# Kernel tuning notes

Hardware: AMD Instinct MI355X
Metric: run time of the kernel (lower is better)

Reference implementation:

```python
import jax, jax.numpy as jnp
import numpy as np

N = 40000          # nodes
E = 400000         # edges (avg degree 10)
MUL0, MUL1 = 64, 32   # 64x0e + 32x1o
RAD, HID = 8, 64      # fc_neurons = [8, 64]
WNUM = 192            # tp.weight_numel = 64+64+32+32
NUM_NEIGHBORS = 10.0
INV3 = 1.0 / np.sqrt(3.0)   # wigner coeff for 1o x 1o -> 0e


def _lin(s, v, Ws, Wv, attr):
    """FullyConnectedTensorProduct(x, 1x0e attr) == per-irrep linear, fan-in normalized."""
    out_s = (s @ Ws) * attr * (1.0 / np.sqrt(Ws.shape[0]))
    out_v = jnp.einsum('nud,uv->nvd', v, Wv) * attr[..., None] * (1.0 / np.sqrt(Wv.shape[0]))
    return out_s, out_v


def setup_inputs() -> dict:
    key = jax.random.key(0)
    ks = jax.random.split(key, 16)
    return {
        'node_input':   jax.random.normal(ks[0], (N, MUL0 + 3 * MUL1), jnp.float32),
        'node_attr':    jnp.ones((N, 1), jnp.float32),
        'edge_attr':    jax.random.normal(ks[1], (E, 4), jnp.float32),   # 1x0e + 1x1o
        'edge_scalars': jax.random.uniform(ks[2], (E, RAD), jnp.float32),
        'W_sc_s': jax.random.normal(ks[3], (MUL0, MUL0), jnp.float32),
        'W_sc_v': jax.random.normal(ks[4], (MUL1, MUL1), jnp.float32),
        'W1_s':   jax.random.normal(ks[5], (MUL0, MUL0), jnp.float32),
        'W1_v':   jax.random.normal(ks[6], (MUL1, MUL1), jnp.float32),
        'W2_s':   jax.random.normal(ks[7], (MUL0 + MUL1, MUL0), jnp.float32),
        'W2_v':   jax.random.normal(ks[8], (MUL0 + MUL1, MUL1), jnp.float32),
        'W3':     jax.random.normal(ks[9], (MUL0 + MUL1, 1), jnp.float32),
        'fcW1':   jax.random.normal(ks[10], (RAD, HID), jnp.float32),
        'fcW2':   jax.random.normal(ks[11], (HID, WNUM), jnp.float32),
        'edge_src': jax.random.randint(ks[12], (E,), 0, N, jnp.int32),
        'edge_dst': jax.random.randint(ks[13], (E,), 0, N, jnp.int32),
    }


def reference(node_input, node_attr, edge_attr, edge_scalars,
              W_sc_s, W_sc_v, W1_s, W1_v, W2_s, W2_v, W3, fcW1, fcW2,
              edge_src, edge_dst):
    n = node_input.shape[0]
    s_in = node_input[:, :MUL0]                       # (N, 64)   0e
    v_in = node_input[:, MUL0:].reshape(n, MUL1, 3)   # (N, 32,3) 1o

    # self connection + first linear (FCTP with 1x0e attr)
    sc_s, sc_v = _lin(s_in, v_in, W_sc_s, W_sc_v, node_attr)
    f_s,  f_v  = _lin(s_in, v_in, W1_s,  W1_v,  node_attr)

    # radial MLP -> per-edge tensor-product weights (silu, fan-in normalized)
    h = jax.nn.silu(edge_scalars @ fcW1 * (1.0 / np.sqrt(RAD)))
    w = h @ fcW2 * (1.0 / np.sqrt(HID))               # (E, 192)
    wA, wB, wC, wD = w[:, :64], w[:, 64:128], w[:, 128:160], w[:, 160:192]

    # gather source node features
    xs = f_s[edge_src]                                # (E, 64)
    xv = f_v[edge_src]                                # (E, 32, 3)
    y0 = edge_attr[:, :1]                             # (E, 1)  0e
    y1 = edge_attr[:, 1:4]                            # (E, 3)  1o

    # 'uvu' tensor-product paths -> irreps_mid = 64x0e + 32x0e + 64x1o + 32x1o
    outA = wA * xs * y0                                            # 0e x 0e -> 0e
    outD = wD * jnp.einsum('eud,ed->eu', xv, y1) * INV3            # 1o x 1o -> 0e
    outB = wB[:, :, None] * xs[:, :, None] * y1[:, None, :]       # 0e x 1o -> 1o
    outC = wC[:, :, None] * xv * y0[:, :, None]                    # 1o x 0e -> 1o
    edge_feat = jnp.concatenate(
        [outA, outD, outB.reshape(-1, MUL0 * 3), outC.reshape(-1, MUL1 * 3)], axis=1)  # (E, 384)

    # scatter_add into destination nodes, normalized by sqrt(num_neighbors)
    agg = jax.ops.segment_sum(edge_feat, edge_dst, num_segments=n)
    agg = agg * (1.0 / np.sqrt(NUM_NEIGHBORS))

    ms = agg[:, :MUL0 + MUL1]                               # (N, 96)   0e
    mv = agg[:, MUL0 + MUL1:].reshape(n, MUL0 + MUL1, 3)    # (N, 96,3) 1o

    # lin2: mid -> output ; lin3: mid -> 0e (scalars only)
    c_s, c_v = _lin(ms, mv, W2_s, W2_v, node_attr)
    conv = jnp.concatenate([c_s, c_v.reshape(n, -1)], axis=1)
    sc   = jnp.concatenate([sc_s, sc_v.reshape(n, -1)], axis=1)
    angle = 0.1 * (ms @ W3) * node_attr * (1.0 / np.sqrt(MUL0 + MUL1))  # (N, 1)

    # sc.output_mask is all-ones here (every output irrep has a path)
    cos, sin = jnp.cos(angle), jnp.sin(angle)
    return cos * sc + sin * conv
```

## Files before the change

kernel.cpp:

```cpp
#include <hip/hip_runtime.h>
#include <math.h>

#define MUL0 64
#define MUL1 32
#define RADF 8
#define HIDF 64
#define WNUM 192
#define NODE_F 160
#define AGG_F  384

#define INV_SQRT64 0.125f
#define INV_SQRT32 0.17677669529663687f
#define INV_SQRT8  0.35355339059327373f
#define INV_SQRT96 0.10206207261596575f
#define INV_SQRT10 0.31622776601683794f
#define INV_SQRT3  0.5773502691896258f

typedef __attribute__((ext_vector_type(8))) short bf16x8;
typedef __attribute__((ext_vector_type(4))) float f32x4;

__device__ __forceinline__ float bf2f(unsigned short u) {
    return __uint_as_float((unsigned)u << 16);
}
__device__ __forceinline__ unsigned short f2bfu(float x) {
    unsigned ua = __float_as_uint(x);
    return (unsigned short)((ua + 0x7FFF + ((ua >> 16) & 1)) >> 16);
}
__device__ __forceinline__ unsigned bf16pack(float a, float b) {
    unsigned ua = __float_as_uint(a);
    unsigned ub = __float_as_uint(b);
    ua = (ua + 0x7FFF + ((ua >> 16) & 1)) >> 16;
    ub = (ub + 0x7FFF + ((ub >> 16) & 1)) >> 16;
    return ua | (ub << 16);
}
__device__ __forceinline__ int rdlane(int v, int i) {
    return __builtin_amdgcn_readlane(v, i);
}
__device__ __forceinline__ float rdlanef(float v, int i) {
    return __int_as_float(__builtin_amdgcn_readlane(__float_as_int(v), i));
}
__device__ __forceinline__ bf16x8 cvt8(float4 a, float4 b) {
    union { unsigned q[4]; bf16x8 v; } r;
    r.q[0] = bf16pack(a.x, a.y);
    r.q[1] = bf16pack(a.z, a.w);
    r.q[2] = bf16pack(b.x, b.y);
    r.q[3] = bf16pack(b.z, b.w);
    return r.v;
}

__global__ __launch_bounds__(256) void k_node_lin(
    const float* __restrict__ node_input,
    const float* __restrict__ node_attr,
    const float* __restrict__ W1_s,
    const float* __restrict__ W1_v,
    float* __restrict__ f, int N)
{
    __shared__ unsigned short s_w1s[8 * 64 * 8];
    __shared__ unsigned short s_w1v[4 * 32 * 8];
    int tid = threadIdx.x;

    for (int task = tid; task < 8 * 64; task += 256) {
        int col = task & 63, koct = task >> 6;
        const float* wp = W1_s + (size_t)(koct * 8) * MUL0 + col;
        unsigned pk0 = bf16pack(wp[0 * MUL0] * INV_SQRT64, wp[1 * MUL0] * INV_SQRT64);
        unsigned pk1 = bf16pack(wp[2 * MUL0] * INV_SQRT64, wp[3 * MUL0] * INV_SQRT64);
        unsigned pk2 = bf16pack(wp[4 * MUL0] * INV_SQRT64, wp[5 * MUL0] * INV_SQRT64);
        unsigned pk3 = bf16pack(wp[6 * MUL0] * INV_SQRT64, wp[7 * MUL0] * INV_SQRT64);
        *(uint4*)&s_w1s[task * 8] = make_uint4(pk0, pk1, pk2, pk3);
    }
    for (int task = tid; task < 4 * 32; task += 256) {
        int col = task & 31, koct = task >> 5;
        const float* wp = W1_v + (size_t)(koct * 8) * MUL1 + col;
        unsigned pk0 = bf16pack(wp[0 * MUL1] * INV_SQRT32, wp[1 * MUL1] * INV_SQRT32);
        unsigned pk1 = bf16pack(wp[2 * MUL1] * INV_SQRT32, wp[3 * MUL1] * INV_SQRT32);
        unsigned pk2 = bf16pack(wp[4 * MUL1] * INV_SQRT32, wp[5 * MUL1] * INV_SQRT32);
        unsigned pk3 = bf16pack(wp[6 * MUL1] * INV_SQRT32, wp[7 * MUL1] * INV_SQRT32);
        *(uint4*)&s_w1v[task * 8] = make_uint4(pk0, pk1, pk2, pk3);
    }
    __syncthreads();

    int lane = tid & 63;
    int wv = tid >> 6;
    int l15 = lane & 15, lh = lane >> 4;
    int ntiles = (N + 15) >> 4;

    for (int tile = blockIdx.x * 4 + wv; tile < ntiles; tile += gridDim.x * 4) {
        int n0 = tile << 4;
        int m = min(16, N - n0);
        int nrow = n0 + min(l15, m - 1);
        const float* inn = node_input + (size_t)nrow * NODE_F;

        float attr[4];
        #pragma unroll
        for (int r = 0; r < 4; ++r)
            attr[r] = node_attr[n0 + min(lh * 4 + r, m - 1)];

        bf16x8 inS[2];
        #pragma unroll
        for (int kk = 0; kk < 2; ++kk) {
            const float* p0 = inn + kk * 32 + lh * 8;
            inS[kk] = cvt8(*(const float4*)p0, *(const float4*)(p0 + 4));
        }
        #pragma unroll
        for (int cb = 0; cb < 4; ++cb) {
            f32x4 a = {0.f, 0.f, 0.f, 0.f};
            #pragma unroll
            for (int kk = 0; kk < 2; ++kk) {
                bf16x8 b = *(const bf16x8*)&s_w1s[(((kk * 4 + lh) * 64) + cb * 16 + l15) * 8];
                a = __builtin_amdgcn_mfma_f32_16x16x32_bf16(inS[kk], b, a, 0, 0, 0);
            }
            #pragma unroll
            for (int r = 0; r < 4; ++r) {
                int node = lh * 4 + r;
                if (node < m)
                    f[(size_t)(n0 + node) * NODE_F + cb * 16 + l15] = a[r] * attr[r];
            }
        }

        #pragma unroll
        for (int d = 0; d < 3; ++d) {
            float t[8];
            #pragma unroll
            for (int j = 0; j < 8; ++j)
                t[j] = inn[64 + (lh * 8 + j) * 3 + d];
            bf16x8 inV = cvt8(make_float4(t[0], t[1], t[2], t[3]),
                              make_float4(t[4], t[5], t[6], t[7]));
            #pragma unroll
            for (int cb = 0; cb < 2; ++cb) {
                bf16x8 b = *(const bf16x8*)&s_w1v[((lh * 32) + cb * 16 + l15) * 8];
                f32x4 a = {0.f, 0.f, 0.f, 0.f};
                a = __builtin_amdgcn_mfma_f32_16x16x32_bf16(inV, b, a, 0, 0, 0);
                #pragma unroll
                for (int r = 0; r < 4; ++r) {
                    int node = lh * 4 + r;
                    if (node < m)
                        f[(size_t)(n0 + node) * NODE_F + 64 + d * 32 + cb * 16 + l15] =
                            a[r] * attr[r];
                }
            }
        }
    }
}

__global__ void k_count(const int* __restrict__ edge_dst, int* deg, int E)
{
    int e = blockIdx.x * blockDim.x + threadIdx.x;
    if (e < E) atomicAdd(&deg[edge_dst[e]], 1);
}

__global__ __launch_bounds__(1024) void k_scan(const int* __restrict__ deg,
                                               int* __restrict__ off,
                                               int* __restrict__ cur, int N)
{
    __shared__ int swsum[16];
    __shared__ int swoff[16];
    __shared__ int sbase;
    __shared__ int stotal;
    int lane = threadIdx.x & 63, wid = threadIdx.x >> 6;
    if (threadIdx.x == 0) sbase = 0;
    __syncthreads();
    int ngroups = N >> 2;
    for (int base = 0; base < ngroups; base += 1024) {
        int g = base + threadIdx.x;
        int4 v = make_int4(0, 0, 0, 0);
        if (g < ngroups) v = ((const int4*)deg)[g];
        int s = v.x + v.y + v.z + v.w;
        int val = s;
        #pragma unroll
        for (int sh = 1; sh < 64; sh <<= 1) {
            int t = __shfl_up(val, sh);
            if (lane >= sh) val += t;
        }
        if (lane == 63) swsum[wid] = val;
        __syncthreads();
        if (threadIdx.x < 16) {
            int x = swsum[threadIdx.x];
            int xv = x;
            #pragma unroll
            for (int sh = 1; sh < 16; sh <<= 1) {
                int t = __shfl_up(xv, sh);
                if ((int)threadIdx.x >= sh) xv += t;
            }
            swoff[threadIdx.x] = xv - x;
            if (threadIdx.x == 15) stotal = xv;
        }
        __syncthreads();
        if (g < ngroups) {
            int b = sbase + swoff[wid] + (val - s);
            int4 o;
            o.x = b; o.y = b + v.x; o.z = o.y + v.y; o.w = o.z + v.z;
            ((int4*)off)[g] = o;
            ((int4*)cur)[g] = o;
        }
        __syncthreads();
        if (threadIdx.x == 0) sbase += stotal;
        __syncthreads();
    }
    if (threadIdx.x == 0) {
        int b = sbase;
        for (int i = (ngroups << 2); i < N; ++i) { off[i] = b; cur[i] = b; b += deg[i]; }
        off[N] = b;
    }
}

__global__ void k_scatter(const int* __restrict__ edge_dst,
                          int* cur, int* __restrict__ csr, int E)
{
    int e = blockIdx.x * blockDim.x + threadIdx.x;
    if (e < E) {
        int d = edge_dst[e];
        int pos = atomicAdd(&cur[d], 1);
        csr[pos] = e;
    }
}

#define FLUSH_AGG(node)                                              \
    do {                                                             \
        float* an = agg + (size_t)(node) * AGG_F;                    \
        atomicAdd(&an[lane], accA);                                  \
        atomicAdd(&an[96  + lane], accB0);                           \
        atomicAdd(&an[192 + lane], accB1);                           \
        atomicAdd(&an[288 + lane], accB2);                           \
        if (lane < 32) {                                             \
            atomicAdd(&an[160 + u], accX0);                          \
            atomicAdd(&an[256 + u], accX1);                          \
            atomicAdd(&an[352 + u], accX2);                          \
        } else {                                                     \
            atomicAdd(&an[64 + u], accX0);                           \
        }                                                            \
    } while (0)

__global__ __launch_bounds__(256, 3) void k_edge_fused(
    const float* __restrict__ f,
    const float* __restrict__ edge_scalars,
    const float* __restrict__ edge_attr,
    const float* __restrict__ fcW1,
    const float* __restrict__ fcW2,
    const int* __restrict__ edge_src,
    const int* __restrict__ edge_dst,
    const int* __restrict__ csr,
    float* agg, int E)
{
    __shared__ unsigned short s_w2t[8 * 192 * 8];
    __shared__ unsigned short s_w[4][16 * 216];
    __shared__ float s_fcW1[512];

    int tid  = threadIdx.x;
    int lane = tid & 63;
    int wv   = tid >> 6;
    int l15  = lane & 15, lh = lane >> 4;
    int u    = lane & 31;

    for (int task = tid; task < 1536; task += 256) {
        int col = task % 192, oct = task / 192;
        const float* wp = fcW2 + (size_t)(oct * 8) * WNUM + col;
        unsigned pk0 = bf16pack(wp[0 * WNUM], wp[1 * WNUM]);
        unsigned pk1 = bf16pack(wp[2 * WNUM], wp[3 * WNUM]);
        unsigned pk2 = bf16pack(wp[4 * WNUM], wp[5 * WNUM]);
        unsigned pk3 = bf16pack(wp[6 * WNUM], wp[7 * WNUM]);
        *(uint4*)&s_w2t[oct * 1536 + col * 8] = make_uint4(pk0, pk1, pk2, pk3);
    }
    for (int i = tid; i < 512; i += 256)
        s_fcW1[i] = fcW1[i];
    __syncthreads();

    unsigned short* sw = s_w[wv];
    int nwt = (E + 15) >> 4;
    int stride4 = gridDim.x * 4;

    int wt = blockIdx.x * 4 + wv;
    if (wt >= nwt) return;

    int P = wt << 4;
    int m = min(16, E - P);
    int e0 = csr[P + min(l15, m - 1)];
    int src = edge_src[e0];
    int dst = edge_dst[e0];
    float4 ea = *(const float4*)(edge_attr + (size_t)e0 * 4);
    float4 es0, es1;
    {
        const float4* esp = (const float4*)(edge_scalars + (size_t)e0 * RADF);
        es0 = esp[0]; es1 = esp[1];
    }

    while (true) {
        int wt_n = wt + stride4;
        bool hn = wt_n < nwt;
        int P_n = hn ? (wt_n << 4) : 0;
        int m_n = hn ? min(16, E - P_n) : 1;

        int e_n = csr[hn ? (P_n + min(l15, m_n - 1)) : 0];

        float xs[16], xv0[16], xv1[16], xv2[16];
        #pragma unroll
        for (int i = 0; i < 16; ++i) {
            int si = rdlane(src, i);
            const float* fb = f + (size_t)si * NODE_F;
            xs[i]  = fb[lane];
            xv0[i] = fb[64 + u];
            xv1[i] = fb[96 + u];
            xv2[i] = fb[128 + u];
        }

        float es[8] = {es0.x, es0.y, es0.z, es0.w, es1.x, es1.y, es1.z, es1.w};
        union { unsigned q[4]; bf16x8 v; } A0, A1;
        #pragma unroll
        for (int jp = 0; jp < 4; ++jp) {
            int k0 = lh * 8 + 2 * jp;
            float aL0 = 0.f, aL1 = 0.f, aH0 = 0.f, aH1 = 0.f;
            #pragma unroll
            for (int r = 0; r < 8; ++r) {
                float2 wl = *(const float2*)&s_fcW1[r * 64 + k0];
                float2 wh = *(const float2*)&s_fcW1[r * 64 + 32 + k0];
                aL0 = fmaf(es[r], wl.x, aL0);
                aL1 = fmaf(es[r], wl.y, aL1);
                aH0 = fmaf(es[r], wh.x, aH0);
                aH1 = fmaf(es[r], wh.y, aH1);
            }
            aL0 *= INV_SQRT8; aL1 *= INV_SQRT8; aH0 *= INV_SQRT8; aH1 *= INV_SQRT8;
            aL0 = aL0 / (1.f + __expf(-aL0));
            aL1 = aL1 / (1.f + __expf(-aL1));
            aH0 = aH0 / (1.f + __expf(-aH0));
            aH1 = aH1 / (1.f + __expf(-aH1));
            A0.q[jp] = bf16pack(aL0, aL1);
            A1.q[jp] = bf16pack(aH0, aH1);
        }

        int src_n = edge_src[e_n];
        int dst_n = edge_dst[e_n];
        float4 ea_n = *(const float4*)(edge_attr + (size_t)e_n * 4);
        float4 es0_n, es1_n;
        {
            const float4* espn = (const float4*)(edge_scalars + (size_t)e_n * RADF);
            es0_n = espn[0]; es1_n = espn[1];
        }

        #pragma unroll
        for (int cb = 0; cb < 12; ++cb) {
            bf16x8 b0 = *(const bf16x8*)&s_w2t[ lh      * 1536 + (cb * 16 + l15) * 8];
            bf16x8 b1 = *(const bf16x8*)&s_w2t[(4 + lh) * 1536 + (cb * 16 + l15) * 8];
            f32x4 acc = {0.f, 0.f, 0.f, 0.f};
            acc = __builtin_amdgcn_mfma_f32_16x16x32_bf16(A0.v, b0, acc, 0, 0, 0);
            acc = __builtin_amdgcn_mfma_f32_16x16x32_bf16(A1.v, b1, acc, 0, 0, 0);
            #pragma unroll
            for (int r = 0; r < 4; ++r)
                sw[(lh * 4 + r) * 216 + cb * 16 + l15] = f2bfu(acc[r] * INV_SQRT64);
        }

        float accA = 0.f, accB0 = 0.f, accB1 = 0.f, accB2 = 0.f;
        float accX0 = 0.f, accX1 = 0.f, accX2 = 0.f;
        int curd = rdlane(dst, 0);
        #pragma unroll
        for (int i = 0; i < 16; ++i) {
            if (i < m) {
                int di = rdlane(dst, i);
                if (di != curd) {
                    FLUSH_AGG(curd);
                    accA = accB0 = accB1 = accB2 = 0.f;
                    accX0 = accX1 = accX2 = 0.f;
                    curd = di;
                }
                float eax = rdlanef(ea.x, i);
                float eay = rdlanef(ea.y, i);
                float eaz = rdlanef(ea.z, i);
                float eaw = rdlanef(ea.w, i);
                float W0 = bf2f(sw[i * 216 + lane]);
                float W1 = bf2f(sw[i * 216 + 64 + lane]);
                float W2 = bf2f(sw[i * 216 + 128 + lane]);
                accA = fmaf(W0 * xs[i], eax, accA);
                float bx = W1 * xs[i];
                accB0 = fmaf(bx, eay, accB0);
                accB1 = fmaf(bx, eaz, accB1);
                accB2 = fmaf(bx, eaw, accB2);
                if (lane < 32) {
                    float cc = W2 * eax;
                    accX0 = fmaf(cc, xv0[i], accX0);
                    accX1 = fmaf(cc, xv1[i], accX1);
                    accX2 = fmaf(cc, xv2[i], accX2);
                } else {
                    float dv = xv0[i] * eay + xv1[i] * eaz + xv2[i] * eaw;
                    accX0 = fmaf(W2 * INV_SQRT3, dv, accX0);
                }
            }
        }
        FLUSH_AGG(curd);

        if (!hn) break;
        wt = wt_n; P = P_n; m = m_n;
        src = src_n; dst = dst_n; ea = ea_n; es0 = es0_n; es1 = es1_n;
    }
}

__global__ __launch_bounds__(256) void k_out(
    const float* __restrict__ node_input,
    const float* __restrict__ node_attr,
    const float* __restrict__ agg,
    const float* __restrict__ W_sc_s,
    const float* __restrict__ W_sc_v,
    const float* __restrict__ W2_s,
    const float* __restrict__ W2_v,
    const float* __restrict__ W3,
    float* __restrict__ out, int N)
{
    __shared__ unsigned short s_w2s[12 * 64 * 8];
    __shared__ unsigned short s_wss[ 8 * 64 * 8];
    __shared__ unsigned short s_w2v[12 * 32 * 8];
    __shared__ unsigned short s_wsv[ 4 * 32 * 8];
    __shared__ unsigned short s_w3 [12 * 16 * 8];

    const float pre = INV_SQRT10 * INV_SQRT96;
    int tid = threadIdx.x;

    for (int task = tid; task < 12 * 64; task += 256) {
        int col = task & 63, koct = task >> 6;
        const float* wp = W2_s + (size_t)(koct * 8) * MUL0 + col;
        unsigned pk0 = bf16pack(wp[0 * MUL0] * pre, wp[1 * MUL0] * pre);
        unsigned pk1 = bf16pack(wp[2 * MUL0] * pre, wp[3 * MUL0] * pre);
        unsigned pk2 = bf16pack(wp[4 * MUL0] * pre, wp[5 * MUL0] * pre);
        unsigned pk3 = bf16pack(wp[6 * MUL0] * pre, wp[7 * MUL0] * pre);
        *(uint4*)&s_w2s[task * 8] = make_uint4(pk0, pk1, pk2, pk3);
    }
    for (int task = tid; task < 8 * 64; task += 256) {
        int col = task & 63, koct = task >> 6;
        const float* wp = W_sc_s + (size_t)(koct * 8) * MUL0 + col;
        unsigned pk0 = bf16pack(wp[0 * MUL0] * INV_SQRT64, wp[1 * MUL0] * INV_SQRT64);
        unsigned pk1 = bf16pack(wp[2 * MUL0] * INV_SQRT64, wp[3 * MUL0] * INV_SQRT64);
        unsigned pk2 = bf16pack(wp[4 * MUL0] * INV_SQRT64, wp[5 * MUL0] * INV_SQRT64);
        unsigned pk3 = bf16pack(wp[6 * MUL0] * INV_SQRT64, wp[7 * MUL0] * INV_SQRT64);
        *(uint4*)&s_wss[task * 8] = make_uint4(pk0, pk1, pk2, pk3);
    }
    for (int task = tid; task < 12 * 32; task += 256) {
        int col = task & 31, koct = task >> 5;
        const float* wp = W2_v + (size_t)(koct * 8) * MUL1 + col;
        unsigned pk0 = bf16pack(wp[0 * MUL1] * pre, wp[1 * MUL1] * pre);
        unsigned pk1 = bf16pack(wp[2 * MUL1] * pre, wp[3 * MUL1] * pre);
        unsigned pk2 = bf16pack(wp[4 * MUL1] * pre, wp[5 * MUL1] * pre);
        unsigned pk3 = bf16pack(wp[6 * MUL1] * pre, wp[7 * MUL1] * pre);
        *(uint4*)&s_w2v[task * 8] = make_uint4(pk0, pk1, pk2, pk3);
    }
    for (int task = tid; task < 4 * 32; task += 256) {
        int col = task & 31, koct = task >> 5;
        const float* wp = W_sc_v + (size_t)(koct * 8) * MUL1 + col;
        unsigned pk0 = bf16pack(wp[0 * MUL1] * INV_SQRT32, wp[1 * MUL1] * INV_SQRT32);
        unsigned pk1 = bf16pack(wp[2 * MUL1] * INV_SQRT32, wp[3 * MUL1] * INV_SQRT32);
        unsigned pk2 = bf16pack(wp[4 * MUL1] * INV_SQRT32, wp[5 * MUL1] * INV_SQRT32);
        unsigned pk3 = bf16pack(wp[6 * MUL1] * INV_SQRT32, wp[7 * MUL1] * INV_SQRT32);
        *(uint4*)&s_wsv[task * 8] = make_uint4(pk0, pk1, pk2, pk3);
    }
    for (int task = tid; task < 12 * 16; task += 256) {
        int col = task & 15, koct = task >> 4;
        const float sc3 = 0.1f * pre;
        unsigned pk0 = 0, pk1 = 0, pk2 = 0, pk3 = 0;
        if (col == 0) {
            const float* wp = W3 + koct * 8;
            pk0 = bf16pack(wp[0] * sc3, wp[1] * sc3);
            pk1 = bf16pack(wp[2] * sc3, wp[3] * sc3);
            pk2 = bf16pack(wp[4] * sc3, wp[5] * sc3);
            pk3 = bf16pack(wp[6] * sc3, wp[7] * sc3);
        }
        *(uint4*)&s_w3[task * 8] = make_uint4(pk0, pk1, pk2, pk3);
    }
    __syncthreads();

    int lane = tid & 63;
    int wv = tid >> 6;
    int l15 = lane & 15, lh = lane >> 4;
    int ntiles = (N + 15) >> 4;

    for (int tile = blockIdx.x * 4 + wv; tile < ntiles; tile += gridDim.x * 4) {
        int n0 = tile << 4;
        int m = min(16, N - n0);
        int nrow = n0 + min(l15, m - 1);
        const float* agn = agg + (size_t)nrow * AGG_F;
        const float* inn = node_input + (size_t)nrow * NODE_F;

        bf16x8 aggA[3], inS[2];
        #pragma unroll
        for (int kk = 0; kk < 3; ++kk) {
            const float* p0 = agn + kk * 32 + lh * 8;
            aggA[kk] = cvt8(*(const float4*)p0, *(const float4*)(p0 + 4));
        }
        #pragma unroll
        for (int kk = 0; kk < 2; ++kk) {
            const float* p0 = inn + kk * 32 + lh * 8;
            inS[kk] = cvt8(*(const float4*)p0, *(const float4*)(p0 + 4));
        }

        f32x4 convS[4], scS[4], angD = {0.f, 0.f, 0.f, 0.f};
        #pragma unroll
        for (int cb = 0; cb < 4; ++cb) {
            f32x4 a = {0.f, 0.f, 0.f, 0.f};
            #pragma unroll
            for (int kk = 0; kk < 3; ++kk) {
                bf16x8 b = *(const bf16x8*)&s_w2s[(((kk * 4 + lh) * 64) + cb * 16 + l15) * 8];
                a = __builtin_amdgcn_mfma_f32_16x16x32_bf16(aggA[kk], b, a, 0, 0, 0);
            }
            convS[cb] = a;
            f32x4 s = {0.f, 0.f, 0.f, 0.f};
            #pragma unroll
            for (int kk = 0; kk < 2; ++kk) {
                bf16x8 b = *(const bf16x8*)&s_wss[(((kk * 4 + lh) * 64) + cb * 16 + l15) * 8];
                s = __builtin_amdgcn_mfma_f32_16x16x32_bf16(inS[kk], b, s, 0, 0, 0);
            }
            scS[cb] = s;
        }
        #pragma unroll
        for (int kk = 0; kk < 3; ++kk) {
            bf16x8 b = *(const bf16x8*)&s_w3[(((kk * 4 + lh) * 16) + l15) * 8];
            angD = __builtin_amdgcn_mfma_f32_16x16x32_bf16(aggA[kk], b, angD, 0, 0, 0);
        }

        float attr[4], cs[4], sn[4];
        #pragma unroll
        for (int r = 0; r < 4; ++r) {
            attr[r] = node_attr[n0 + min(lh * 4 + r, m - 1)];
            float ang = __shfl(angD[r], lane & 48) * attr[r];
            cs[r] = cosf(ang);
            sn[r] = sinf(ang);
        }

        #pragma unroll
        for (int cb = 0; cb < 4; ++cb)
            #pragma unroll
            for (int r = 0; r < 4; ++r) {
                int node = lh * 4 + r;
                if (node < m)
                    out[(size_t)(n0 + node) * NODE_F + cb * 16 + l15] =
                        attr[r] * (cs[r] * scS[cb][r] + sn[r] * convS[cb][r]);
            }

        #pragma unroll
        for (int d = 0; d < 3; ++d) {
            bf16x8 aggV[3], inV;
            #pragma unroll
            for (int kk = 0; kk < 3; ++kk) {
                const float* p0 = agn + 96 + d * 96 + kk * 32 + lh * 8;
                aggV[kk] = cvt8(*(const float4*)p0, *(const float4*)(p0 + 4));
            }
            {
                float t[8];
                #pragma unroll
                for (int j = 0; j < 8; ++j)
                    t[j] = inn[64 + (lh * 8 + j) * 3 + d];
                inV = cvt8(make_float4(t[0], t[1], t[2], t[3]),
                           make_float4(t[4], t[5], t[6], t[7]));
            }
            #pragma unroll
            for (int cb = 0; cb < 2; ++cb) {
                f32x4 a = {0.f, 0.f, 0.f, 0.f};
                #pragma unroll
                for (int kk = 0; kk < 3; ++kk) {
                    bf16x8 b = *(const bf16x8*)&s_w2v[(((kk * 4 + lh) * 32) + cb * 16 + l15) * 8];
                    a = __builtin_amdgcn_mfma_f32_16x16x32_bf16(aggV[kk], b, a, 0, 0, 0);
                }
                f32x4 s = {0.f, 0.f, 0.f, 0.f};
                {
                    bf16x8 b = *(const bf16x8*)&s_wsv[((lh * 32) + cb * 16 + l15) * 8];
                    s = __builtin_amdgcn_mfma_f32_16x16x32_bf16(inV, b, s, 0, 0, 0);
                }
                #pragma unroll
                for (int r = 0; r < 4; ++r) {
                    int node = lh * 4 + r;
                    if (node < m)
                        out[(size_t)(n0 + node) * NODE_F + 64 + (cb * 16 + l15) * 3 + d] =
                            attr[r] * (cs[r] * s[r] + sn[r] * a[r]);
                }
            }
        }
    }
}

extern "C" void kernel_launch(void* const* d_in, const int* in_sizes, int n_in,
                              void* d_out, int out_size, void* d_ws, size_t ws_size,
                              hipStream_t stream)
{
    const float* node_input   = (const float*)d_in[0];
    const float* node_attr    = (const float*)d_in[1];
    const float* edge_attr    = (const float*)d_in[2];
    const float* edge_scalars = (const float*)d_in[3];
    const float* W_sc_s       = (const float*)d_in[4];
    const float* W_sc_v       = (const float*)d_in[5];
    const float* W1_s         = (const float*)d_in[6];
    const float* W1_v         = (const float*)d_in[7];
    const float* W2_s         = (const float*)d_in[8];
    const float* W2_v         = (const float*)d_in[9];
    const float* W3           = (const float*)d_in[10];
    const float* fcW1         = (const float*)d_in[11];
    const float* fcW2         = (const float*)d_in[12];
    const int*   edge_src     = (const int*)d_in[13];
    const int*   edge_dst     = (const int*)d_in[14];
    float* out = (float*)d_out;

    const int N = in_sizes[1];
    const int E = in_sizes[13];

    char* p = (char*)d_ws;
    float* agg = (float*)p;  p += (size_t)N * AGG_F * sizeof(float);
    int*   deg = (int*)p;    p += (size_t)N * sizeof(int);
    int*   cur = (int*)p;    p += (size_t)N * sizeof(int);
    int*   csr = (int*)p;    p += (size_t)E * sizeof(int);
    int*   off = (int*)p;    p += (size_t)(N + 1) * sizeof(int);

    float* f = out;

    hipMemsetAsync(deg, 0, (size_t)N * sizeof(int), stream);
    hipMemsetAsync(agg, 0, (size_t)N * AGG_F * sizeof(float), stream);

    int eb = (E + 255) / 256;
    k_count<<<eb, 256, 0, stream>>>(edge_dst, deg, E);
    k_scan<<<1, 1024, 0, stream>>>(deg, off, cur, N);
    k_scatter<<<eb, 256, 0, stream>>>(edge_dst, cur, csr, E);

    int ntiles = (N + 15) / 16;
    int gridL = (ntiles + 3) / 4;
    k_node_lin<<<gridL, 256, 0, stream>>>(node_input, node_attr, W1_s, W1_v, f, N);

    int nwt = (E + 15) / 16;
    int gridF = (nwt + 3) / 4;
    if (gridF > 1536) gridF = 1536;
    k_edge_fused<<<gridF, 256, 0, stream>>>(f, edge_scalars, edge_attr, fcW1, fcW2,
                                            edge_src, edge_dst, csr, agg, E);

    int gridO = (ntiles + 3) / 4;
    if (gridO > 640) gridO = 640;
    k_out<<<gridO, 256, 0, stream>>>(node_input, node_attr, agg,
                                     W_sc_s, W_sc_v, W2_s, W2_v, W3, out, N);
}
```

Measured before the change: 244.4 us.

## Store node features in bf16 and use plain stores for tile-owned destination nodes

Node-linear output f is now stored as bf16 in a separate workspace buffer, halving the bytes read by the random per-edge source gathers in the edge kernel. Edge tiles also read the CSR offsets to tell whether a destination node's edges lie entirely inside the current 16-edge tile. If so, the accumulated row is written with plain stores instead of atomics, and atomics are kept only for nodes that span tile boundaries. This cuts atomic traffic to agg but adds two offset loads per tile and reduces the precision of the gathered features.

```diff
diff --git a/kernel.cpp b/kernel.cpp
--- a/kernel.cpp
+++ b/kernel.cpp
@@ -53,7 +53,7 @@
     const float* __restrict__ node_attr,
     const float* __restrict__ W1_s,
     const float* __restrict__ W1_v,
-    float* __restrict__ f, int N)
+    unsigned short* __restrict__ f, int N)
 {
     __shared__ unsigned short s_w1s[8 * 64 * 8];
     __shared__ unsigned short s_w1v[4 * 32 * 8];
@@ -113,7 +113,7 @@
             for (int r = 0; r < 4; ++r) {
                 int node = lh * 4 + r;
                 if (node < m)
-                    f[(size_t)(n0 + node) * NODE_F + cb * 16 + l15] = a[r] * attr[r];
+                    f[(size_t)(n0 + node) * NODE_F + cb * 16 + l15] = f2bfu(a[r] * attr[r]);
             }
         }
 
@@ -135,7 +135,7 @@
                     int node = lh * 4 + r;
                     if (node < m)
                         f[(size_t)(n0 + node) * NODE_F + 64 + d * 32 + cb * 16 + l15] =
-                            a[r] * attr[r];
+                            f2bfu(a[r] * attr[r]);
                 }
             }
         }
@@ -214,24 +214,38 @@
     }
 }
 
-#define FLUSH_AGG(node)                                              \
+#define FLUSH_AGG(node, AT)                                          \
     do {                                                             \
         float* an = agg + (size_t)(node) * AGG_F;                    \
-        atomicAdd(&an[lane], accA);                                  \
-        atomicAdd(&an[96  + lane], accB0);                           \
-        atomicAdd(&an[192 + lane], accB1);                           \
-        atomicAdd(&an[288 + lane], accB2);                           \
-        if (lane < 32) {                                             \
-            atomicAdd(&an[160 + u], accX0);                          \
-            atomicAdd(&an[256 + u], accX1);                          \
-            atomicAdd(&an[352 + u], accX2);                          \
+        if (AT) {                                                    \
+            atomicAdd(&an[lane], accA);                              \
+            atomicAdd(&an[96  + lane], accB0);                       \
+            atomicAdd(&an[192 + lane], accB1);                       \
+            atomicAdd(&an[288 + lane], accB2);                       \
+            if (lane < 32) {                                         \
+                atomicAdd(&an[160 + u], accX0);                      \
+                atomicAdd(&an[256 + u], accX1);                      \
+                atomicAdd(&an[352 + u], accX2);                      \
+            } else {                                                 \
+                atomicAdd(&an[64 + u], accX0);                       \
+            }                                                        \
         } else {                                                     \
-            atomicAdd(&an[64 + u], accX0);                           \
+            an[lane] = accA;                                         \
+            an[96  + lane] = accB0;                                  \
+            an[192 + lane] = accB1;                                  \
+            an[288 + lane] = accB2;                                  \
+            if (lane < 32) {                                         \
+                an[160 + u] = accX0;                                 \
+                an[256 + u] = accX1;                                 \
+                an[352 + u] = accX2;                                 \
+            } else {                                                 \
+                an[64 + u] = accX0;                                  \
+            }                                                        \
         }                                                            \
     } while (0)
 
 __global__ __launch_bounds__(256, 3) void k_edge_fused(
-    const float* __restrict__ f,
+    const unsigned short* __restrict__ f,
     const float* __restrict__ edge_scalars,
     const float* __restrict__ edge_attr,
     const float* __restrict__ fcW1,
@@ -239,6 +253,7 @@
     const int* __restrict__ edge_src,
     const int* __restrict__ edge_dst,
     const int* __restrict__ csr,
+    const int* __restrict__ off,
     float* agg, int E)
 {
     __shared__ unsigned short s_w2t[8 * 192 * 8];
@@ -284,6 +299,11 @@
     }
 
     while (true) {
+        int firstd = rdlane(dst, 0);
+        int lastd  = rdlane(dst, m - 1);
+        int off_first = off[firstd];
+        int off_last  = off[lastd + 1];
+
         int wt_n = wt + stride4;
         bool hn = wt_n < nwt;
         int P_n = hn ? (wt_n << 4) : 0;
@@ -295,11 +315,11 @@
         #pragma unroll
         for (int i = 0; i < 16; ++i) {
             int si = rdlane(src, i);
-            const float* fb = f + (size_t)si * NODE_F;
-            xs[i]  = fb[lane];
-            xv0[i] = fb[64 + u];
-            xv1[i] = fb[96 + u];
-            xv2[i] = fb[128 + u];
+            const unsigned short* fb = f + (size_t)si * NODE_F;
+            xs[i]  = bf2f(fb[lane]);
+            xv0[i] = bf2f(fb[64 + u]);
+            xv1[i] = bf2f(fb[96 + u]);
+            xv2[i] = bf2f(fb[128 + u]);
         }
 
         float es[8] = {es0.x, es0.y, es0.z, es0.w, es1.x, es1.y, es1.z, es1.w};
@@ -355,7 +375,8 @@
             if (i < m) {
                 int di = rdlane(dst, i);
                 if (di != curd) {
-                    FLUSH_AGG(curd);
+                    bool at = (curd == firstd) && (off_first < P);
+                    FLUSH_AGG(curd, at);
                     accA = accB0 = accB1 = accB2 = 0.f;
                     accX0 = accX1 = accX2 = 0.f;
                     curd = di;
@@ -383,7 +404,10 @@
                 }
             }
         }
-        FLUSH_AGG(curd);
+        {
+            bool at_fin = ((curd == firstd) && (off_first < P)) || (off_last > P + m);
+            FLUSH_AGG(curd, at_fin);
+        }
 
         if (!hn) break;
         wt = wt_n; P = P_n; m = m_n;
@@ -595,13 +619,12 @@
     const int E = in_sizes[13];
 
     char* p = (char*)d_ws;
-    float* agg = (float*)p;  p += (size_t)N * AGG_F * sizeof(float);
-    int*   deg = (int*)p;    p += (size_t)N * sizeof(int);
-    int*   cur = (int*)p;    p += (size_t)N * sizeof(int);
-    int*   csr = (int*)p;    p += (size_t)E * sizeof(int);
-    int*   off = (int*)p;    p += (size_t)(N + 1) * sizeof(int);
-
-    float* f = out;
+    float* agg = (float*)p;            p += (size_t)N * AGG_F * sizeof(float);
+    unsigned short* fbf = (unsigned short*)p;  p += (size_t)N * NODE_F * sizeof(unsigned short);
+    int*   deg = (int*)p;              p += (size_t)N * sizeof(int);
+    int*   cur = (int*)p;              p += (size_t)N * sizeof(int);
+    int*   csr = (int*)p;              p += (size_t)E * sizeof(int);
+    int*   off = (int*)p;              p += (size_t)(N + 1) * sizeof(int);
 
     hipMemsetAsync(deg, 0, (size_t)N * sizeof(int), stream);
     hipMemsetAsync(agg, 0, (size_t)N * AGG_F * sizeof(float), stream);
@@ -613,13 +636,13 @@
 
     int ntiles = (N + 15) / 16;
     int gridL = (ntiles + 3) / 4;
-    k_node_lin<<<gridL, 256, 0, stream>>>(node_input, node_attr, W1_s, W1_v, f, N);
+    k_node_lin<<<gridL, 256, 0, stream>>>(node_input, node_attr, W1_s, W1_v, fbf, N);
 
     int nwt = (E + 15) / 16;
     int gridF = (nwt + 3) / 4;
     if (gridF > 1536) gridF = 1536;
-    k_edge_fused<<<gridF, 256, 0, stream>>>(f, edge_scalars, edge_attr, fcW1, fcW2,
-                                            edge_src, edge_dst, csr, agg, E);
+    k_edge_fused<<<gridF, 256, 0, stream>>>(fbf, edge_scalars, edge_attr, fcW1, fcW2,
+                                            edge_src, edge_dst, csr, off, agg, E);
 
     int gridO = (ntiles + 3) / 4;
     if (gridO > 640) gridO = 640;
```

Measured after the change: 239.1 us. -2.1%, faster.
